# Kernel tuning notes

Hardware: AMD Instinct MI355X
Metric: run time of the kernel (lower is better)

## Reference

```python
import jax, jax.numpy as jnp
import numpy as np

N = 100000          # num nodes
E = 1_600_000       # num edges
D = 128             # in_channels
H = 128             # hidden_channels
NUM_LAYERS = 3


def setup_inputs() -> dict:
    key = jax.random.key(0)
    ks = jax.random.split(key, 6)
    return {
        "emb": jax.random.normal(ks[0], (N, D), dtype=jnp.float32),
        "w1": jax.random.normal(ks[1], (H, D), dtype=jnp.float32) / np.sqrt(D).astype(np.float32),
        "b1": jnp.zeros((H,), jnp.float32),
        "w2": jax.random.normal(ks[2], (H, H), dtype=jnp.float32) / np.sqrt(H).astype(np.float32),
        "b2": jnp.zeros((H,), jnp.float32),
        "eps": jnp.zeros((NUM_LAYERS,), jnp.float32),  # learn_eps=True, init 0 per layer
        "edge_w": jax.random.uniform(ks[3], (E,), dtype=jnp.float32),
        "src": jax.random.randint(ks[4], (E,), 0, N, dtype=jnp.int32),
        "dst": jax.random.randint(ks[5], (E,), 0, N, dtype=jnp.int32),
    }


def _gin_layer(x, src, dst, edge_w, deg_inv, eps, W, b):
    # DGL GINConv(mean, edge_weight): msg = x[src] * w ; agg = mean over in-edges (divide by in-degree)
    msg = x[src] * edge_w[:, None]                                  # [E, d]
    agg = jax.ops.segment_sum(msg, dst, num_segments=N) * deg_inv[:, None]
    return ((1.0 + eps) * x + agg) @ W.T + b


def reference(emb, w1, b1, w2, b2, eps, edge_w, src, dst):
    # in-degree (count of in-edges), zero-degree nodes get 0 aggregation
    deg = jax.ops.segment_sum(jnp.ones((E,), jnp.float32), dst, num_segments=N)
    deg_inv = jnp.where(deg > 0, 1.0 / jnp.maximum(deg, 1.0), 0.0)

    x = _gin_layer(emb, src, dst, edge_w, deg_inv, eps[0], w1, b1)
    x = jax.nn.relu(x)  # dropout is identity in eval mode
    for i in range(1, NUM_LAYERS - 1):
        x = _gin_layer(x, src, dst, edge_w, deg_inv, eps[i], w2, b2)  # lin2 shared
        x = jax.nn.relu(x)
    x = _gin_layer(x, src, dst, edge_w, deg_inv, eps[NUM_LAYERS - 1], w2, b2)
    x = x.at[0].set(jnp.zeros((x.shape[1],), x.dtype))  # x[0] = zeros
    return x
```

## Files before the change

### kernel.cpp

```cpp
#include <hip/hip_runtime.h>
#include <hip/hip_bf16.h>

#define N_NODES 100000
#define N_EDGES 1600000
#define DIM 128
#define SCAN_CHUNK 1024

typedef __attribute__((ext_vector_type(8))) short bf16x8;
typedef __attribute__((ext_vector_type(4))) float f32x4;
typedef __attribute__((ext_vector_type(4))) short bf16x4;

__device__ __forceinline__ float b2f(short s) {
    return __uint_as_float(((unsigned int)(unsigned short)s) << 16);
}

__global__ void cvtall_kernel(const float* __restrict__ emb, const float* __restrict__ w1,
                              const float* __restrict__ w2, __hip_bfloat16* __restrict__ embb,
                              __hip_bfloat16* __restrict__ w1b, __hip_bfloat16* __restrict__ w2b) {
    const int n4e = N_NODES * DIM / 4;
    const int n4w = DIM * DIM / 4;
    int i = blockIdx.x * blockDim.x + threadIdx.x;
    const float* in;
    __hip_bfloat16* out;
    int j;
    if (i < n4e) { in = emb; out = embb; j = i; }
    else if (i < n4e + n4w) { in = w1; out = w1b; j = i - n4e; }
    else if (i < n4e + 2 * n4w) { in = w2; out = w2b; j = i - n4e - n4w; }
    else return;
    f32x4 v = ((const f32x4*)in)[j];
    bf16x4 o;
    o.x = (short)__bfloat16_as_ushort(__float2bfloat16(v.x));
    o.y = (short)__bfloat16_as_ushort(__float2bfloat16(v.y));
    o.z = (short)__bfloat16_as_ushort(__float2bfloat16(v.z));
    o.w = (short)__bfloat16_as_ushort(__float2bfloat16(v.w));
    ((bf16x4*)out)[j] = o;
}

__global__ __launch_bounds__(256) void degrank_kernel(const int* __restrict__ dst,
                                                      int* __restrict__ deg,
                                                      int* __restrict__ rank) {
    const int S = 2048 * 256;
    int tid = blockIdx.x * blockDim.x + threadIdx.x;
    int e3 = tid + 3 * S;
    int d0 = dst[tid];
    int d1 = dst[tid + S];
    int d2 = dst[tid + 2 * S];
    int d3 = (e3 < N_EDGES) ? dst[e3] : -1;
    int r0 = atomicAdd(&deg[d0], 1);
    int r1 = atomicAdd(&deg[d1], 1);
    int r2 = atomicAdd(&deg[d2], 1);
    int r3 = (d3 >= 0) ? atomicAdd(&deg[d3], 1) : 0;
    rank[tid] = r0;
    rank[tid + S] = r1;
    rank[tid + 2 * S] = r2;
    if (e3 < N_EDGES) rank[e3] = r3;
}

__global__ void scan1_kernel(const int* __restrict__ deg, int* __restrict__ bsum) {
    __shared__ int s[256];
    int t = threadIdx.x;
    int base = blockIdx.x * SCAN_CHUNK + t * 4;
    int v = 0;
    for (int k = 0; k < 4; k++) { int i = base + k; if (i < N_NODES) v += deg[i]; }
    s[t] = v;
    __syncthreads();
    for (int off = 128; off > 0; off >>= 1) { if (t < off) s[t] += s[t + off]; __syncthreads(); }
    if (t == 0) bsum[blockIdx.x] = s[0];
}

__global__ void scan2_kernel(const int* __restrict__ bsum, int* __restrict__ bscan,
                             int* __restrict__ row_start, int nb) {
    if (threadIdx.x == 0) {
        int run = 0;
        for (int b = 0; b < nb; b++) { bscan[b] = run; run += bsum[b]; }
        row_start[N_NODES] = run;
    }
}

__global__ void scan3_kernel(const int* __restrict__ deg, const int* __restrict__ bscan,
                             int* __restrict__ row_start) {
    __shared__ int s[256];
    int t = threadIdx.x;
    int base = blockIdx.x * SCAN_CHUNK + t * 4;
    int v[4]; int tot = 0;
    for (int k = 0; k < 4; k++) { int i = base + k; v[k] = (i < N_NODES) ? deg[i] : 0; tot += v[k]; }
    s[t] = tot;
    __syncthreads();
    for (int off = 1; off < 256; off <<= 1) {
        int a = (t >= off) ? s[t - off] : 0;
        __syncthreads();
        s[t] += a;
        __syncthreads();
    }
    int run = s[t] - tot + bscan[blockIdx.x];
    for (int k = 0; k < 4; k++) {
        int i = base + k;
        if (i < N_NODES) row_start[i] = run;
        run += v[k];
    }
}

#define FI_UNROLL 4
__global__ void fill_kernel(const int* __restrict__ src, const int* __restrict__ dst,
                            const float* __restrict__ ew, const int* __restrict__ rank,
                            const int* __restrict__ row_start, int2* __restrict__ sw_s) {
    int tid = blockIdx.x * blockDim.x + threadIdx.x;
    int nthreads = gridDim.x * blockDim.x;
    int d_[FI_UNROLL], r_[FI_UNROLL], s_[FI_UNROLL], w_[FI_UNROLL], rs_[FI_UNROLL];
#pragma unroll
    for (int k = 0; k < FI_UNROLL; k++) {
        int e = tid + k * nthreads;
        if (e < N_EDGES) {
            d_[k] = dst[e]; r_[k] = rank[e]; s_[k] = src[e] << 8; w_[k] = __float_as_int(ew[e]);
        } else d_[k] = -1;
    }
#pragma unroll
    for (int k = 0; k < FI_UNROLL; k++)
        if (d_[k] >= 0) rs_[k] = row_start[d_[k]];
#pragma unroll
    for (int k = 0; k < FI_UNROLL; k++)
        if (d_[k] >= 0) sw_s[rs_[k] + r_[k]] = make_int2(s_[k], w_[k]);
}

template <int RELU, int ZERO0, int OUTBF>
__global__ __launch_bounds__(256) void aggmm_kernel(const __hip_bfloat16* __restrict__ x,
                                                    const int* __restrict__ row_start,
                                                    const int2* __restrict__ sw_s,
                                                    const float* __restrict__ eps, int li,
                                                    const __hip_bfloat16* __restrict__ W,
                                                    const float* __restrict__ bias,
                                                    void* __restrict__ outv) {
    __shared__ int2 s_sw[4][66];
    __shared__ __hip_bfloat162 s_h[16][64];
    int wv = threadIdx.x >> 6;
    int lane = threadIdx.x & 63;
    int row0 = blockIdx.x * 16;
    int c = lane & 31;
    int half = lane >> 5;
    const char* xb = (const char*)x + (c << 3);
    float ep = 1.0f + eps[li];

    for (int jj = 0; jj < 4; jj++) {
        int j = wv * 4 + jj;
        int n = row0 + j;
        int beg = row_start[n], end = row_start[n + 1];
        float a0 = 0.f, a1 = 0.f, a2 = 0.f, a3 = 0.f;
        for (int base = beg; base < end; base += 64) {
            int cnt = min(64, end - base);
            if (lane < cnt) s_sw[wv][lane] = sw_s[base + lane];
            else if (lane == cnt) s_sw[wv][lane] = make_int2(0, 0);
            asm volatile("s_waitcnt lgkmcnt(0)" ::: "memory");
            int cnt2 = (cnt + 1) & ~1;
            int i = 0;
            for (; i + 4 <= cnt2; i += 4) {
                int2 ea = s_sw[wv][i + half];
                int2 eb = s_sw[wv][i + 2 + half];
                bf16x4 va = *(const bf16x4*)(xb + ea.x);
                bf16x4 vb = *(const bf16x4*)(xb + eb.x);
                float wa = __int_as_float(ea.y), wb = __int_as_float(eb.y);
                a0 += b2f(va.x) * wa + b2f(vb.x) * wb;
                a1 += b2f(va.y) * wa + b2f(vb.y) * wb;
                a2 += b2f(va.z) * wa + b2f(vb.z) * wb;
                a3 += b2f(va.w) * wa + b2f(vb.w) * wb;
            }
            for (; i < cnt2; i += 2) {
                int2 e = s_sw[wv][i + half];
                bf16x4 v = *(const bf16x4*)(xb + e.x);
                float w = __int_as_float(e.y);
                a0 += b2f(v.x) * w;
                a1 += b2f(v.y) * w;
                a2 += b2f(v.z) * w;
                a3 += b2f(v.w) * w;
            }
            asm volatile("" ::: "memory");
        }
        a0 += __shfl_xor(a0, 32, 64);
        a1 += __shfl_xor(a1, 32, 64);
        a2 += __shfl_xor(a2, 32, 64);
        a3 += __shfl_xor(a3, 32, 64);
        if (half == 0) {
            int degn = end - beg;
            float dinv = degn > 0 ? 1.0f / (float)degn : 0.0f;
            bf16x4 xs = *(const bf16x4*)((const char*)x + (size_t)n * 256 + (c << 3));
            bf16x4 o;
            o.x = (short)__bfloat16_as_ushort(__float2bfloat16(ep * b2f(xs.x) + a0 * dinv));
            o.y = (short)__bfloat16_as_ushort(__float2bfloat16(ep * b2f(xs.y) + a1 * dinv));
            o.z = (short)__bfloat16_as_ushort(__float2bfloat16(ep * b2f(xs.z) + a2 * dinv));
            o.w = (short)__bfloat16_as_ushort(__float2bfloat16(ep * b2f(xs.w) + a3 * dinv));
            int co = (c * 8) ^ ((j & 7) << 4);
            *(bf16x4*)((char*)&s_h[j][0] + co) = o;
        }
    }
    __syncthreads();

    int lr = lane & 15;
    int kg = lane >> 4;
    bf16x8 a[4];
#pragma unroll
    for (int k = 0; k < 4; k++) {
        int cb = (kg * 16 + k * 64) ^ ((lr & 7) << 4);
        a[k] = *(const bf16x8*)((const char*)&s_h[lr][0] + cb);
    }
    __syncthreads();

    f32x4 acc[2];
#pragma unroll
    for (int t = 0; t < 2; t++) {
        int jt = wv * 2 + t;
        const short* Wp = (const short*)W + (size_t)(jt * 16 + lr) * DIM + kg * 8;
        f32x4 cc = {0.f, 0.f, 0.f, 0.f};
#pragma unroll
        for (int k = 0; k < 4; k++) {
            bf16x8 b = *(const bf16x8*)(Wp + k * 32);
            cc = __builtin_amdgcn_mfma_f32_16x16x32_bf16(a[k], b, cc, 0, 0, 0);
        }
        acc[t] = cc;
    }

    int colb = lane & 15;
    int rb = (lane >> 4) * 4;
    if (OUTBF) {
#pragma unroll
        for (int t = 0; t < 2; t++) {
            int col = (wv * 2 + t) * 16 + colb;
            float bv = bias[col];
#pragma unroll
            for (int r = 0; r < 4; r++) {
                int row = rb + r;
                float v = acc[t][r] + bv;
                if (RELU) v = fmaxf(v, 0.f);
                if (ZERO0 && blockIdx.x == 0 && row == 0) v = 0.f;
                int bo = (row * 256 + col * 2) ^ ((row & 7) << 4);
                *(__hip_bfloat16*)((char*)s_h + bo) = __float2bfloat16(v);
            }
        }
        __syncthreads();
        int row = threadIdx.x >> 4, c16 = threadIdx.x & 15;
        int bo = (row * 256 + c16 * 16) ^ ((row & 7) << 4);
        bf16x8 vv = *(const bf16x8*)((const char*)s_h + bo);
        *(bf16x8*)((char*)outv + (size_t)(row0 + row) * 256 + c16 * 16) = vv;
    } else {
#pragma unroll
        for (int t = 0; t < 2; t++) {
            int col = (wv * 2 + t) * 16 + colb;
            float bv = bias[col];
#pragma unroll
            for (int r = 0; r < 4; r++) {
                int grow = row0 + rb + r;
                float v = acc[t][r] + bv;
                if (RELU) v = fmaxf(v, 0.f);
                if (ZERO0 && grow == 0) v = 0.f;
                ((float*)outv)[(size_t)grow * DIM + col] = v;
            }
        }
    }
}

extern "C" void kernel_launch(void* const* d_in, const int* in_sizes, int n_in,
                              void* d_out, int out_size, void* d_ws, size_t ws_size,
                              hipStream_t stream) {
    const float* emb = (const float*)d_in[0];
    const float* w1  = (const float*)d_in[1];
    const float* b1  = (const float*)d_in[2];
    const float* w2  = (const float*)d_in[3];
    const float* b2  = (const float*)d_in[4];
    const float* eps = (const float*)d_in[5];
    const float* ew  = (const float*)d_in[6];
    const int* src   = (const int*)d_in[7];
    const int* dst   = (const int*)d_in[8];
    float* out = (float*)d_out;

    char* base = (char*)d_ws;
    size_t off = 0;
    auto alloc = [&](size_t bytes) -> char* {
        char* p = base + off;
        off += (bytes + 255) & ~(size_t)255;
        return p;
    };
    int* deg            = (int*)alloc((size_t)N_NODES * 4);
    int* row_start      = (int*)alloc((size_t)(N_NODES + 1) * 4);
    int* rank           = (int*)alloc((size_t)N_EDGES * 4);
    int* bsum           = (int*)alloc(128 * 4);
    int* bscan          = (int*)alloc(128 * 4);
    int2* sw_s          = (int2*)alloc((size_t)N_EDGES * 8);
    __hip_bfloat16* xb  = (__hip_bfloat16*)alloc((size_t)N_NODES * DIM * 2);
    __hip_bfloat16* xc  = (__hip_bfloat16*)alloc((size_t)N_NODES * DIM * 2);
    __hip_bfloat16* embb= (__hip_bfloat16*)alloc((size_t)N_NODES * DIM * 2);
    __hip_bfloat16* w1b = (__hip_bfloat16*)alloc(DIM * DIM * 2);
    __hip_bfloat16* w2b = (__hip_bfloat16*)alloc(DIM * DIM * 2);

    hipMemsetAsync(deg, 0, (size_t)N_NODES * 4, stream);

    {
        int n4 = N_NODES * DIM / 4 + 2 * (DIM * DIM / 4);
        cvtall_kernel<<<(n4 + 255) / 256, 256, 0, stream>>>(emb, w1, w2, embb, w1b, w2b);
    }

    degrank_kernel<<<2048, 256, 0, stream>>>(dst, deg, rank);
    int nb = (N_NODES + SCAN_CHUNK - 1) / SCAN_CHUNK;
    scan1_kernel<<<nb, 256, 0, stream>>>(deg, bsum);
    scan2_kernel<<<1, 64, 0, stream>>>(bsum, bscan, row_start, nb);
    scan3_kernel<<<nb, 256, 0, stream>>>(deg, bscan, row_start);
    {
        int nthreads = ((N_EDGES + FI_UNROLL - 1) / FI_UNROLL + 255) & ~255;
        fill_kernel<<<nthreads / 256, 256, 0, stream>>>(src, dst, ew, rank, row_start, sw_s);
    }

    int blocks = N_NODES / 16;
    aggmm_kernel<1, 0, 1><<<blocks, 256, 0, stream>>>(embb, row_start, sw_s, eps, 0, w1b, b1, xb);
    aggmm_kernel<1, 0, 1><<<blocks, 256, 0, stream>>>(xb,   row_start, sw_s, eps, 1, w2b, b2, xc);
    aggmm_kernel<0, 1, 0><<<blocks, 256, 0, stream>>>(xc,   row_start, sw_s, eps, 2, w2b, b2, out);
}
```

Baseline: 498.0 us.

## Interleave gather of four destination rows per wave to raise memory-level parallelism

Each wave now loads the edge lists and self features for all four of its destination nodes up front and gathers neighbors for the four rows in one interleaved loop, instead of handling the rows one after another. This is meant to keep more independent gather loads in flight and hide latency on the memory-bound aggregation, with rows longer than 64 edges handled in a separate tail loop. The cost is more registers (a 4x4 accumulator array plus more shared memory for edge lists), which may lower occupancy. Shorter rows also waste lanes because the loop runs to the longest of the four rows, reading padded zero entries.

```diff
diff --git a/kernel.cpp b/kernel.cpp
--- a/kernel.cpp
+++ b/kernel.cpp
@@ -130,7 +130,7 @@
                                                     const __hip_bfloat16* __restrict__ W,
                                                     const float* __restrict__ bias,
                                                     void* __restrict__ outv) {
-    __shared__ int2 s_sw[4][66];
+    __shared__ int2 s_sw[4][4][64];
     __shared__ __hip_bfloat162 s_h[16][64];
     int wv = threadIdx.x >> 6;
     int lane = threadIdx.x & 63;
@@ -140,55 +140,89 @@
     const char* xb = (const char*)x + (c << 3);
     float ep = 1.0f + eps[li];
 
-    for (int jj = 0; jj < 4; jj++) {
-        int j = wv * 4 + jj;
-        int n = row0 + j;
-        int beg = row_start[n], end = row_start[n + 1];
-        float a0 = 0.f, a1 = 0.f, a2 = 0.f, a3 = 0.f;
-        for (int base = beg; base < end; base += 64) {
-            int cnt = min(64, end - base);
-            if (lane < cnt) s_sw[wv][lane] = sw_s[base + lane];
-            else if (lane == cnt) s_sw[wv][lane] = make_int2(0, 0);
-            asm volatile("s_waitcnt lgkmcnt(0)" ::: "memory");
-            int cnt2 = (cnt + 1) & ~1;
-            int i = 0;
-            for (; i + 4 <= cnt2; i += 4) {
-                int2 ea = s_sw[wv][i + half];
-                int2 eb = s_sw[wv][i + 2 + half];
-                bf16x4 va = *(const bf16x4*)(xb + ea.x);
-                bf16x4 vb = *(const bf16x4*)(xb + eb.x);
-                float wa = __int_as_float(ea.y), wb = __int_as_float(eb.y);
-                a0 += b2f(va.x) * wa + b2f(vb.x) * wb;
-                a1 += b2f(va.y) * wa + b2f(vb.y) * wb;
-                a2 += b2f(va.z) * wa + b2f(vb.z) * wb;
-                a3 += b2f(va.w) * wa + b2f(vb.w) * wb;
+    int n0 = row0 + wv * 4;
+    int beg[4], cnt[4];
+#pragma unroll
+    for (int j = 0; j < 4; j++) {
+        beg[j] = row_start[n0 + j];
+        cnt[j] = row_start[n0 + j + 1] - beg[j];
+    }
+
+    bf16x4 xs[4];
+#pragma unroll
+    for (int j = 0; j < 4; j++)
+        xs[j] = *(const bf16x4*)((const char*)x + (size_t)(n0 + j) * 256 + (c << 3));
+    int2 er[4];
+#pragma unroll
+    for (int j = 0; j < 4; j++) {
+        er[j] = make_int2(0, 0);
+        if (lane < cnt[j]) er[j] = sw_s[beg[j] + lane];
+    }
+#pragma unroll
+    for (int j = 0; j < 4; j++) s_sw[wv][j][lane] = er[j];
+    asm volatile("s_waitcnt lgkmcnt(0)" ::: "memory");
+
+    float acc[4][4] = {};
+    int cmax = max(max(cnt[0], cnt[1]), max(cnt[2], cnt[3]));
+    int c0 = min(cmax, 64);
+    int c02 = (c0 + 1) & ~1;
+#pragma unroll 2
+    for (int i = 0; i < c02; i += 2) {
+#pragma unroll
+        for (int j = 0; j < 4; j++) {
+            int2 e = s_sw[wv][j][i + half];
+            bf16x4 v = *(const bf16x4*)(xb + e.x);
+            float w = __int_as_float(e.y);
+            acc[j][0] += b2f(v.x) * w;
+            acc[j][1] += b2f(v.y) * w;
+            acc[j][2] += b2f(v.z) * w;
+            acc[j][3] += b2f(v.w) * w;
+        }
+    }
+    asm volatile("" ::: "memory");
+
+    if (cmax > 64) {
+#pragma unroll 1
+        for (int j = 0; j < 4; j++) {
+            int nd = cnt[j];
+#pragma unroll 1
+            for (int base = 64; base < nd; base += 64) {
+                int cc = min(64, nd - base);
+                int2 er2 = make_int2(0, 0);
+                if (lane < cc) er2 = sw_s[beg[j] + base + lane];
+                s_sw[wv][j][lane] = er2;
+                asm volatile("s_waitcnt lgkmcnt(0)" ::: "memory");
+                int cc2 = (cc + 1) & ~1;
+                for (int i = 0; i < cc2; i += 2) {
+                    int2 e = s_sw[wv][j][i + half];
+                    bf16x4 v = *(const bf16x4*)(xb + e.x);
+                    float w = __int_as_float(e.y);
+                    acc[j][0] += b2f(v.x) * w;
+                    acc[j][1] += b2f(v.y) * w;
+                    acc[j][2] += b2f(v.z) * w;
+                    acc[j][3] += b2f(v.w) * w;
+                }
+                asm volatile("" ::: "memory");
             }
-            for (; i < cnt2; i += 2) {
-                int2 e = s_sw[wv][i + half];
-                bf16x4 v = *(const bf16x4*)(xb + e.x);
-                float w = __int_as_float(e.y);
-                a0 += b2f(v.x) * w;
-                a1 += b2f(v.y) * w;
-                a2 += b2f(v.z) * w;
-                a3 += b2f(v.w) * w;
-            }
-            asm volatile("" ::: "memory");
-        }
-        a0 += __shfl_xor(a0, 32, 64);
-        a1 += __shfl_xor(a1, 32, 64);
-        a2 += __shfl_xor(a2, 32, 64);
-        a3 += __shfl_xor(a3, 32, 64);
+        }
+    }
+
+#pragma unroll
+    for (int j = 0; j < 4; j++) {
+        float a0 = acc[j][0] + __shfl_xor(acc[j][0], 32, 64);
+        float a1 = acc[j][1] + __shfl_xor(acc[j][1], 32, 64);
+        float a2 = acc[j][2] + __shfl_xor(acc[j][2], 32, 64);
+        float a3 = acc[j][3] + __shfl_xor(acc[j][3], 32, 64);
         if (half == 0) {
-            int degn = end - beg;
-            float dinv = degn > 0 ? 1.0f / (float)degn : 0.0f;
-            bf16x4 xs = *(const bf16x4*)((const char*)x + (size_t)n * 256 + (c << 3));
+            float dinv = cnt[j] > 0 ? 1.0f / (float)cnt[j] : 0.0f;
             bf16x4 o;
-            o.x = (short)__bfloat16_as_ushort(__float2bfloat16(ep * b2f(xs.x) + a0 * dinv));
-            o.y = (short)__bfloat16_as_ushort(__float2bfloat16(ep * b2f(xs.y) + a1 * dinv));
-            o.z = (short)__bfloat16_as_ushort(__float2bfloat16(ep * b2f(xs.z) + a2 * dinv));
-            o.w = (short)__bfloat16_as_ushort(__float2bfloat16(ep * b2f(xs.w) + a3 * dinv));
-            int co = (c * 8) ^ ((j & 7) << 4);
-            *(bf16x4*)((char*)&s_h[j][0] + co) = o;
+            o.x = (short)__bfloat16_as_ushort(__float2bfloat16(ep * b2f(xs[j].x) + a0 * dinv));
+            o.y = (short)__bfloat16_as_ushort(__float2bfloat16(ep * b2f(xs[j].y) + a1 * dinv));
+            o.z = (short)__bfloat16_as_ushort(__float2bfloat16(ep * b2f(xs[j].z) + a2 * dinv));
+            o.w = (short)__bfloat16_as_ushort(__float2bfloat16(ep * b2f(xs[j].w) + a3 * dinv));
+            int jr = wv * 4 + j;
+            int co = (c * 8) ^ ((jr & 7) << 4);
+            *(bf16x4*)((char*)&s_h[jr][0] + co) = o;
         }
     }
     __syncthreads();
@@ -203,7 +237,7 @@
     }
     __syncthreads();
 
-    f32x4 acc[2];
+    f32x4 accm[2];
 #pragma unroll
     for (int t = 0; t < 2; t++) {
         int jt = wv * 2 + t;
@@ -214,7 +248,7 @@
             bf16x8 b = *(const bf16x8*)(Wp + k * 32);
             cc = __builtin_amdgcn_mfma_f32_16x16x32_bf16(a[k], b, cc, 0, 0, 0);
         }
-        acc[t] = cc;
+        accm[t] = cc;
     }
 
     int colb = lane & 15;
@@ -227,7 +261,7 @@
 #pragma unroll
             for (int r = 0; r < 4; r++) {
                 int row = rb + r;
-                float v = acc[t][r] + bv;
+                float v = accm[t][r] + bv;
                 if (RELU) v = fmaxf(v, 0.f);
                 if (ZERO0 && blockIdx.x == 0 && row == 0) v = 0.f;
                 int bo = (row * 256 + col * 2) ^ ((row & 7) << 4);
@@ -247,7 +281,7 @@
 #pragma unroll
             for (int r = 0; r < 4; r++) {
                 int grow = row0 + rb + r;
-                float v = acc[t][r] + bv;
+                float v = accm[t][r] + bv;
                 if (RELU) v = fmaxf(v, 0.f);
                 if (ZERO0 && grow == 0) v = 0.f;
                 ((float*)outv)[(size_t)grow * DIM + col] = v;
```

After: 458.7 us. 1.09x faster.
